# Kernel tuning notes

Measured on AMD Instinct MI355X. Metric: run time of the kernel, lower is better.

The kernel has to match this reference:

```python
import jax, jax.numpy as jnp
import numpy as np
from jax import lax

EPS = 1e-8


def setup_inputs() -> dict:
    key = jax.random.key(0)
    ks = jax.random.split(key, 8)
    B, Cin, Cout, Wd, H, Wi, K = 16, 512, 512, 512, 64, 64, 3
    x = jax.random.normal(ks[0], (B, Cin, H, Wi), dtype=jnp.float32)
    w = jax.random.normal(ks[1], (B, Wd), dtype=jnp.float32)
    noise = jax.random.normal(ks[2], (B, 1, H, Wi), dtype=jnp.float32)
    # EqualizedLinear params (weight stored as N(0,1), runtime scale 1/sqrt(w_dim)); bias init 1.0
    w_style = jax.random.normal(ks[3], (Cin, Wd), dtype=jnp.float32)
    b_style = jnp.ones((Cin,), dtype=jnp.float32)
    # ConvModLayer equalized weight, stored N(0,1), runtime scale 1/sqrt(Cin*K*K)
    w_conv = jax.random.normal(ks[4], (Cout, Cin, K, K), dtype=jnp.float32)
    scale_noise = 0.1 * jax.random.normal(ks[5], (1,), dtype=jnp.float32)
    bias = 0.1 * jax.random.normal(ks[6], (Cout,), dtype=jnp.float32)
    return {"x": x, "w": w, "noise": noise, "w_style": w_style, "b_style": b_style,
            "w_conv": w_conv, "scale_noise": scale_noise, "bias": bias}


def reference(x, w, noise, w_style, b_style, w_conv, scale_noise, bias):
    B, Cin, H, W = x.shape
    Cout, _, K, _ = w_conv.shape
    # to_style: equalized linear, A = w @ (w_style / sqrt(w_dim)).T + b_style
    c_lin = 1.0 / jnp.sqrt(jnp.float32(w_style.shape[1]))
    A = w @ (w_style * c_lin).T + b_style  # [B, Cin]
    # modulated conv (equalized conv weight scale)
    c_conv = 1.0 / jnp.sqrt(jnp.float32(Cin * K * K))
    wts = (w_conv * c_conv)[None] * A[:, None, :, None, None]  # [B, Cout, Cin, K, K]
    demod = lax.rsqrt(jnp.sum(wts * wts, axis=(2, 3, 4), keepdims=True) + EPS)
    wts = wts * demod
    # grouped-conv batch trick: groups = B
    xg = x.reshape(1, B * Cin, H, W)
    wg = wts.reshape(B * Cout, Cin, K, K)
    out = lax.conv_general_dilated(xg, wg, (1, 1), 'SAME',
                                   feature_group_count=B,
                                   dimension_numbers=('NCHW', 'OIHW', 'NCHW'))
    out = out.reshape(B, Cout, H, W)
    out = out + scale_noise[None, :, None, None] * noise
    out = out + bias[None, :, None, None]
    return jnp.where(out >= 0, out, 0.2 * out)  # LeakyReLU(0.2)
```

## Files before the change

### kernel.cpp

```cpp
#include <hip/hip_runtime.h>
#include <stdint.h>


typedef __attribute__((ext_vector_type(8))) short s16x8;
typedef __attribute__((ext_vector_type(4))) float f32x4;

constexpr int CIN = 512, COUT = 512, WD = 512, HW = 4096;
constexpr float C_LIN  = 0.04419417382415922f;
constexpr float C_CONV = 0.014731391274719739f;
constexpr float CC2    = 1.0f / 4608.0f;

constexpr int WSEG = 2432;

constexpr size_t WS_A = 0, WS_S = 32768, WS_DM = 1081344;
constexpr size_t WS_WP = 1310720, WS_XT = 6291456;

__device__ __forceinline__ unsigned short f2bf(float f) {
  union { float f; unsigned int u; } v; v.f = f;
  unsigned int u = v.u + 0x7FFFu + ((v.u >> 16) & 1u);
  return (unsigned short)(u >> 16);
}

__device__ __forceinline__ void gload16(const void* g, void* l) {
  __builtin_amdgcn_global_load_lds((const __attribute__((address_space(1))) void*)g,
                                   (__attribute__((address_space(3))) void*)l, 16, 0, 0);
}

__global__ void k_style(const float* __restrict__ w, const float* __restrict__ wsty,
                        const float* __restrict__ bs, float* __restrict__ A) {
  __shared__ float wl[WD];
  __shared__ float red[256];
  const int ci0 = blockIdx.x * 64, b = blockIdx.y, tid = threadIdx.x;
  for (int i = tid; i < WD; i += 256) wl[i] = w[b * WD + i];
  __syncthreads();
  const int ci_l = tid & 63, part = tid >> 6;
  const float4* row = (const float4*)(wsty + (size_t)(ci0 + ci_l) * WD + part * 128);
  float acc = 0.f;
#pragma unroll
  for (int k = 0; k < 32; ++k) {
    float4 v = row[k];
    acc += v.x * wl[part*128 + 4*k] + v.y * wl[part*128 + 4*k+1]
         + v.z * wl[part*128 + 4*k+2] + v.w * wl[part*128 + 4*k+3];
  }
  red[tid] = acc;
  __syncthreads();
  if (part == 0)
    A[b * CIN + ci0 + ci_l] =
        (red[ci_l] + red[64+ci_l] + red[128+ci_l] + red[192+ci_l]) * C_LIN + bs[ci0 + ci_l];
}

__global__ void k_sw(const float* __restrict__ wc, uint4* __restrict__ wp,
                     float* __restrict__ S) {
  __shared__ float wt[64][289];
  const int ct = blockIdx.x, ch = blockIdx.y, tid = threadIdx.x;
  const int co0 = ct * 64, ci0 = ch * 32;
  for (int i = tid; i < 64 * 288; i += 256) {
    int co = i / 288, r = i - co * 288;
    wt[co][r] = wc[(size_t)(co0 + co) * 4608 + (size_t)ci0 * 9 + r];
  }
  __syncthreads();
  uint4* seg = wp + (size_t)(ct * 16 + ch) * WSEG;
  for (int c = tid; c < 2304; c += 256) {
    int t = c >> 8, rem = c & 255, s = rem >> 6, co = rem & 63;
    union { unsigned short u[8]; uint4 v; } pk;
#pragma unroll
    for (int j = 0; j < 8; ++j) pk.u[j] = f2bf(wt[co][(s*8 + j) * 9 + t] * C_CONV);
    seg[(t * 4 + s) * 66 + co] = pk.v;
  }
  for (int i = tid; i < 2048; i += 256) {
    int co = i >> 5, ci = i & 31;
    float s_ = 0.f;
#pragma unroll
    for (int t = 0; t < 9; ++t) { float v = wt[co][ci * 9 + t]; s_ += v * v; }
    S[(size_t)(co0 + co) * CIN + ci0 + ci] = s_;
  }
}

__global__ void k_demod(const float* __restrict__ S, const float* __restrict__ A,
                        float* __restrict__ dm) {
  __shared__ float a2[CIN];
  __shared__ float red[256];
  const int co0 = blockIdx.x * 32, b = blockIdx.y, tid = threadIdx.x;
  for (int i = tid; i < CIN; i += 256) { float a = A[b * CIN + i]; a2[i] = a * a; }
  __syncthreads();
  const int co_l = tid & 31, part = tid >> 5;
  const float4* row = (const float4*)(S + (size_t)(co0 + co_l) * CIN + part * 64);
  float acc = 0.f;
#pragma unroll
  for (int k = 0; k < 16; ++k) {
    float4 v = row[k];
    acc += v.x * a2[part*64 + 4*k] + v.y * a2[part*64 + 4*k+1]
         + v.z * a2[part*64 + 4*k+2] + v.w * a2[part*64 + 4*k+3];
  }
  red[tid] = acc;
  __syncthreads();
  if (tid < 32) {
    float s_ = 0.f;
#pragma unroll
    for (int p = 0; p < 8; ++p) s_ += red[p * 32 + tid];
    dm[b * COUT + co0 + tid] = rsqrtf(CC2 * s_ + 1e-8f);
  }
}

__global__ void k_xt(const float* __restrict__ x, const float* __restrict__ A,
                     uint4* __restrict__ xt) {
  const int wid = (blockIdx.x << 2) + (threadIdx.x >> 6);
  const int lane = threadIdx.x & 63;
  const int row = wid & 63, ch = (wid >> 6) & 15, b = wid >> 10;
  const float* xb = x + ((size_t)(b * CIN + ch * 32) << 12) + (row << 6) + lane;
  const float* Ab = A + b * CIN + ch * 32;
  uint4* dst = xt + (size_t)((b << 4) + ch) * 16896 + (size_t)(row << 2) * 66;
#pragma unroll
  for (int s = 0; s < 4; ++s) {
    union { unsigned short u[8]; uint4 v; } pk;
#pragma unroll
    for (int j = 0; j < 8; ++j)
      pk.u[j] = f2bf(xb[(size_t)(s * 8 + j) << 12] * Ab[s * 8 + j]);
    dst[s * 66 + 1 + lane] = pk.v;
    if (lane < 2) dst[s * 66 + lane * 65] = (uint4){0, 0, 0, 0};
  }
}

__global__ __launch_bounds__(512, 4) void k_conv(
    const uint4* __restrict__ xt, const uint4* __restrict__ wp,
    const float* __restrict__ demod, const float* __restrict__ noise,
    const float* __restrict__ sn_, const float* __restrict__ bias,
    float* __restrict__ out) {

  __shared__ __align__(16) uint4 x_lds[2640];
  __shared__ __align__(16) uint4 w_lds[WSEG];
  __shared__ float dm_l[64], bi_l[64];

  const int sp = blockIdx.x, ct = blockIdx.y, b = blockIdx.z;
  const int r0 = sp * 8, co0 = ct * 64;
  const int tid = threadIdx.x, lane = tid & 63, wave = tid >> 6;
  const int l15 = lane & 15, l4 = lane >> 4;

  if (tid < 64) dm_l[tid] = demod[b * COUT + co0 + tid];
  else if (tid < 128) bi_l[tid - 64] = bias[co0 + tid - 64];
  if (sp == 0) for (int i = tid; i < 264; i += 512) x_lds[i] = (uint4){0, 0, 0, 0};
  if (sp == 7) for (int i = tid; i < 264; i += 512) x_lds[2376 + i] = (uint4){0, 0, 0, 0};

  const int lo = (r0 - 1 > 0) ? r0 - 1 : 0;
  const int hi = (r0 + 8 < 63) ? r0 + 8 : 63;
  const int cells = (hi - lo + 1) * 264;
  const int dst0 = (lo - (r0 - 1)) * 264;
  const int nI = cells >> 6, tail = cells & 63;

  f32x4 acc[4][4];
#pragma unroll
  for (int m = 0; m < 4; ++m)
#pragma unroll
    for (int f = 0; f < 4; ++f) acc[m][f] = (f32x4){0.f, 0.f, 0.f, 0.f};
  __syncthreads();

  for (int ch = 0; ch < 16; ++ch) {
    const uint4* xsrc = xt + ((size_t)(b * 16 + ch) * 64 + lo) * 264;
    const uint4* wsrc = wp + (size_t)(ct * 16 + ch) * WSEG;
    for (int i = wave; i < nI; i += 8)
      gload16(xsrc + i * 64 + lane, &x_lds[dst0 + i * 64]);
    if (tid < tail) x_lds[dst0 + nI * 64 + tid] = xsrc[nI * 64 + tid];
    for (int i = wave; i < 38; i += 8)
      gload16(wsrc + i * 64 + lane, &w_lds[i * 64]);
    __syncthreads();

#pragma unroll
    for (int t = 0; t < 9; ++t) {
      const int dh = t / 3, dw = t - dh * 3;
      s16x8 afr[4], bfr[4];
#pragma unroll
      for (int m = 0; m < 4; ++m)
        afr[m] = *(const s16x8*)&w_lds[(t * 4 + l4) * 66 + m * 16 + l15];
#pragma unroll
      for (int f = 0; f < 4; ++f)
        bfr[f] = *(const s16x8*)&x_lds[((wave + dh) * 4 + l4) * 66 + f * 16 + l15 + dw];
#pragma unroll
      for (int m = 0; m < 4; ++m)
#pragma unroll
        for (int f = 0; f < 4; ++f)
          acc[m][f] = __builtin_amdgcn_mfma_f32_16x16x32_bf16(afr[m], bfr[f], acc[m][f], 0, 0, 0);
    }
    __syncthreads();
  }

  const float sn = sn_[0];
  const int row = r0 + wave;
  float nz[4];
#pragma unroll
  for (int f = 0; f < 4; ++f) nz[f] = sn * noise[b * HW + row * 64 + f * 16 + l15];
#pragma unroll
  for (int m = 0; m < 4; ++m) {
#pragma unroll
    for (int reg = 0; reg < 4; ++reg) {
      const int co_l = m * 16 + l4 * 4 + reg;
      const float d = dm_l[co_l], bv = bi_l[co_l];
      float* op = out + ((size_t)(b * COUT + co0 + co_l)) * HW + row * 64;
#pragma unroll
      for (int f = 0; f < 4; ++f) {
        float v = d * acc[m][f][reg] + nz[f] + bv;
        op[f * 16 + l15] = (v >= 0.f) ? v : 0.2f * v;
      }
    }
  }
}

extern "C" void kernel_launch(void* const* d_in, const int* in_sizes, int n_in,
                              void* d_out, int out_size, void* d_ws, size_t ws_size,
                              hipStream_t stream) {
  (void)in_sizes; (void)n_in; (void)out_size; (void)ws_size;
  const float* x           = (const float*)d_in[0];
  const float* w           = (const float*)d_in[1];
  const float* noise       = (const float*)d_in[2];
  const float* w_style     = (const float*)d_in[3];
  const float* b_style     = (const float*)d_in[4];
  const float* w_conv      = (const float*)d_in[5];
  const float* scale_noise = (const float*)d_in[6];
  const float* bias        = (const float*)d_in[7];
  float* out = (float*)d_out;

  char* ws = (char*)d_ws;
  float* A     = (float*)(ws + WS_A);
  float* S     = (float*)(ws + WS_S);
  float* demod = (float*)(ws + WS_DM);
  uint4* wpack = (uint4*)(ws + WS_WP);
  uint4* xt    = (uint4*)(ws + WS_XT);

  k_style<<<dim3(8, 16), 256, 0, stream>>>(w, w_style, b_style, A);
  k_sw<<<dim3(8, 16), 256, 0, stream>>>(w_conv, wpack, S);
  k_demod<<<dim3(16, 16), 256, 0, stream>>>(S, A, demod);
  k_xt<<<4096, 256, 0, stream>>>(x, A, xt);
  k_conv<<<dim3(8, 8, 16), 512, 0, stream>>>(xt, wpack, demod, noise, scale_noise, bias, out);
}
```

Measured before the change: 494.5 us.

## Double-buffer conv LDS staging and fuse style/demod into neighbouring kernels

The conv kernel now double-buffers the x and weight LDS tiles, prefetching the next channel chunk while MFMAs run on the current one, and raises wave priority around the MFMA block. The style linear is fused into the x-transform kernel (each block recomputes its 32 style values), and the demodulation reduction moves into the conv prologue, dropping two launches. The weight segment padding is removed. In exchange, doubling LDS lowers occupancy (launch bounds go from 4 to 2 blocks per CU), and the style and demod reductions are recomputed redundantly across blocks.

Result: slower. 546.8 us (+10.6%).

```diff
diff --git a/kernel.cpp b/kernel.cpp
--- a/kernel.cpp
+++ b/kernel.cpp
@@ -10,9 +10,9 @@
 constexpr float C_CONV = 0.014731391274719739f;
 constexpr float CC2    = 1.0f / 4608.0f;
 
-constexpr int WSEG = 2432;
-
-constexpr size_t WS_A = 0, WS_S = 32768, WS_DM = 1081344;
+constexpr int WSEG = 2304;
+
+constexpr size_t WS_A = 0, WS_S = 32768;
 constexpr size_t WS_WP = 1310720, WS_XT = 6291456;
 
 __device__ __forceinline__ unsigned short f2bf(float f) {
@@ -24,29 +24,6 @@
 __device__ __forceinline__ void gload16(const void* g, void* l) {
   __builtin_amdgcn_global_load_lds((const __attribute__((address_space(1))) void*)g,
                                    (__attribute__((address_space(3))) void*)l, 16, 0, 0);
-}
-
-__global__ void k_style(const float* __restrict__ w, const float* __restrict__ wsty,
-                        const float* __restrict__ bs, float* __restrict__ A) {
-  __shared__ float wl[WD];
-  __shared__ float red[256];
-  const int ci0 = blockIdx.x * 64, b = blockIdx.y, tid = threadIdx.x;
-  for (int i = tid; i < WD; i += 256) wl[i] = w[b * WD + i];
-  __syncthreads();
-  const int ci_l = tid & 63, part = tid >> 6;
-  const float4* row = (const float4*)(wsty + (size_t)(ci0 + ci_l) * WD + part * 128);
-  float acc = 0.f;
-#pragma unroll
-  for (int k = 0; k < 32; ++k) {
-    float4 v = row[k];
-    acc += v.x * wl[part*128 + 4*k] + v.y * wl[part*128 + 4*k+1]
-         + v.z * wl[part*128 + 4*k+2] + v.w * wl[part*128 + 4*k+3];
-  }
-  red[tid] = acc;
-  __syncthreads();
-  if (part == 0)
-    A[b * CIN + ci0 + ci_l] =
-        (red[ci_l] + red[64+ci_l] + red[128+ci_l] + red[192+ci_l]) * C_LIN + bs[ci0 + ci_l];
 }
 
 __global__ void k_sw(const float* __restrict__ wc, uint4* __restrict__ wp,
@@ -65,7 +42,7 @@
     union { unsigned short u[8]; uint4 v; } pk;
 #pragma unroll
     for (int j = 0; j < 8; ++j) pk.u[j] = f2bf(wt[co][(s*8 + j) * 9 + t] * C_CONV);
-    seg[(t * 4 + s) * 66 + co] = pk.v;
+    seg[(t * 4 + s) * 64 + co] = pk.v;
   }
   for (int i = tid; i < 2048; i += 256) {
     int co = i >> 5, ci = i & 31;
@@ -76,59 +53,68 @@
   }
 }
 
-__global__ void k_demod(const float* __restrict__ S, const float* __restrict__ A,
-                        float* __restrict__ dm) {
-  __shared__ float a2[CIN];
+__global__ __launch_bounds__(256) void k_xta(
+    const float* __restrict__ x, const float* __restrict__ w,
+    const float* __restrict__ wsty, const float* __restrict__ bs,
+    float* __restrict__ A, uint4* __restrict__ xt) {
+  __shared__ float wl[WD];
   __shared__ float red[256];
-  const int co0 = blockIdx.x * 32, b = blockIdx.y, tid = threadIdx.x;
-  for (int i = tid; i < CIN; i += 256) { float a = A[b * CIN + i]; a2[i] = a * a; }
-  __syncthreads();
-  const int co_l = tid & 31, part = tid >> 5;
-  const float4* row = (const float4*)(S + (size_t)(co0 + co_l) * CIN + part * 64);
-  float acc = 0.f;
-#pragma unroll
-  for (int k = 0; k < 16; ++k) {
-    float4 v = row[k];
-    acc += v.x * a2[part*64 + 4*k] + v.y * a2[part*64 + 4*k+1]
-         + v.z * a2[part*64 + 4*k+2] + v.w * a2[part*64 + 4*k+3];
-  }
-  red[tid] = acc;
-  __syncthreads();
-  if (tid < 32) {
-    float s_ = 0.f;
-#pragma unroll
-    for (int p = 0; p < 8; ++p) s_ += red[p * 32 + tid];
-    dm[b * COUT + co0 + tid] = rsqrtf(CC2 * s_ + 1e-8f);
-  }
-}
-
-__global__ void k_xt(const float* __restrict__ x, const float* __restrict__ A,
-                     uint4* __restrict__ xt) {
-  const int wid = (blockIdx.x << 2) + (threadIdx.x >> 6);
-  const int lane = threadIdx.x & 63;
-  const int row = wid & 63, ch = (wid >> 6) & 15, b = wid >> 10;
-  const float* xb = x + ((size_t)(b * CIN + ch * 32) << 12) + (row << 6) + lane;
-  const float* Ab = A + b * CIN + ch * 32;
-  uint4* dst = xt + (size_t)((b << 4) + ch) * 16896 + (size_t)(row << 2) * 66;
-#pragma unroll
-  for (int s = 0; s < 4; ++s) {
-    union { unsigned short u[8]; uint4 v; } pk;
-#pragma unroll
-    for (int j = 0; j < 8; ++j)
-      pk.u[j] = f2bf(xb[(size_t)(s * 8 + j) << 12] * Ab[s * 8 + j]);
-    dst[s * 66 + 1 + lane] = pk.v;
-    if (lane < 2) dst[s * 66 + lane * 65] = (uint4){0, 0, 0, 0};
-  }
-}
-
-__global__ __launch_bounds__(512, 4) void k_conv(
+  __shared__ float As[32];
+  const int p = blockIdx.x, b = blockIdx.y, tid = threadIdx.x;
+  const int ch = p >> 2, rowgrp = p & 3, ci0 = ch * 32;
+  for (int i = tid; i < WD; i += 256) wl[i] = w[b * WD + i];
+  __syncthreads();
+  const int ci_l = tid >> 3, part = tid & 7;
+  {
+    const float4* row = (const float4*)(wsty + (size_t)(ci0 + ci_l) * WD + part * 64);
+    float acc = 0.f;
+#pragma unroll
+    for (int k = 0; k < 16; ++k) {
+      float4 v = row[k];
+      acc += v.x * wl[part*64 + 4*k] + v.y * wl[part*64 + 4*k+1]
+           + v.z * wl[part*64 + 4*k+2] + v.w * wl[part*64 + 4*k+3];
+    }
+    red[tid] = acc;
+  }
+  __syncthreads();
+  if (part == 0) {
+    float s = 0.f;
+#pragma unroll
+    for (int q = 0; q < 8; ++q) s += red[ci_l * 8 + q];
+    float a = s * C_LIN + bs[ci0 + ci_l];
+    As[ci_l] = a;
+    if (rowgrp == 0) A[b * CIN + ci0 + ci_l] = a;
+  }
+  __syncthreads();
+  const int lane = tid & 63, wave = tid >> 6;
+  const float* xb = x + ((size_t)(b * CIN + ci0) << 12) + lane;
+  uint4* dstb = xt + (size_t)((b << 4) + ch) * 16896;
+#pragma unroll
+  for (int i = 0; i < 4; ++i) {
+    const int rw = rowgrp * 16 + wave * 4 + i;
+    const float* xr = xb + (rw << 6);
+    uint4* dst = dstb + (size_t)(rw * 4) * 66;
+#pragma unroll
+    for (int s = 0; s < 4; ++s) {
+      union { unsigned short u[8]; uint4 v; } pk;
+#pragma unroll
+      for (int j = 0; j < 8; ++j)
+        pk.u[j] = f2bf(xr[(size_t)(s * 8 + j) << 12] * As[s * 8 + j]);
+      dst[s * 66 + 1 + lane] = pk.v;
+      if (lane < 2) dst[s * 66 + lane * 65] = (uint4){0, 0, 0, 0};
+    }
+  }
+}
+
+__global__ __launch_bounds__(512, 2) void k_conv(
     const uint4* __restrict__ xt, const uint4* __restrict__ wp,
-    const float* __restrict__ demod, const float* __restrict__ noise,
-    const float* __restrict__ sn_, const float* __restrict__ bias,
-    float* __restrict__ out) {
-
-  __shared__ __align__(16) uint4 x_lds[2640];
-  __shared__ __align__(16) uint4 w_lds[WSEG];
+    const float* __restrict__ S, const float* __restrict__ A,
+    const float* __restrict__ noise, const float* __restrict__ sn_,
+    const float* __restrict__ bias, float* __restrict__ out) {
+
+  __shared__ __align__(16) uint4 x_lds[2][2640];
+  __shared__ __align__(16) uint4 w_lds[2][WSEG];
+  __shared__ float red[512];
   __shared__ float dm_l[64], bi_l[64];
 
   const int sp = blockIdx.x, ct = blockIdx.y, b = blockIdx.z;
@@ -136,33 +122,62 @@
   const int tid = threadIdx.x, lane = tid & 63, wave = tid >> 6;
   const int l15 = lane & 15, l4 = lane >> 4;
 
-  if (tid < 64) dm_l[tid] = demod[b * COUT + co0 + tid];
-  else if (tid < 128) bi_l[tid - 64] = bias[co0 + tid - 64];
-  if (sp == 0) for (int i = tid; i < 264; i += 512) x_lds[i] = (uint4){0, 0, 0, 0};
-  if (sp == 7) for (int i = tid; i < 264; i += 512) x_lds[2376 + i] = (uint4){0, 0, 0, 0};
-
   const int lo = (r0 - 1 > 0) ? r0 - 1 : 0;
   const int hi = (r0 + 8 < 63) ? r0 + 8 : 63;
   const int cells = (hi - lo + 1) * 264;
   const int dst0 = (lo - (r0 - 1)) * 264;
-  const int nI = cells >> 6, tail = cells & 63;
+
+  auto stage = [&](int buf, int ch) {
+    const uint4* xsrc = xt + ((size_t)(b * 16 + ch) * 64 + lo) * 264;
+    for (int i = wave; i * 64 < cells; i += 8)
+      if (i * 64 + lane < cells)
+        gload16(xsrc + i * 64 + lane, &x_lds[buf][dst0 + i * 64]);
+    const uint4* wsrc = wp + (size_t)(ct * 16 + ch) * WSEG;
+    for (int i = wave; i < 36; i += 8)
+      gload16(wsrc + i * 64 + lane, &w_lds[buf][i * 64]);
+  };
+
+  stage(0, 0);
+
+  if (sp == 0) for (int i = tid; i < 264; i += 512) {
+    x_lds[0][i] = (uint4){0,0,0,0}; x_lds[1][i] = (uint4){0,0,0,0};
+  }
+  if (sp == 7) for (int i = tid; i < 264; i += 512) {
+    x_lds[0][2376+i] = (uint4){0,0,0,0}; x_lds[1][2376+i] = (uint4){0,0,0,0};
+  }
+
+  {
+    const int co = tid >> 3, part = tid & 7;
+    const float4* srow = (const float4*)(S + (size_t)(co0 + co) * CIN + part * 64);
+    const float4* arow = (const float4*)(A + (size_t)b * CIN + part * 64);
+    float acc = 0.f;
+#pragma unroll
+    for (int k = 0; k < 16; ++k) {
+      float4 sv = srow[k], av = arow[k];
+      acc += sv.x*av.x*av.x + sv.y*av.y*av.y + sv.z*av.z*av.z + sv.w*av.w*av.w;
+    }
+    red[tid] = acc;
+  }
+  __syncthreads();
+  if (tid < 64) {
+    float s_ = 0.f;
+#pragma unroll
+    for (int q = 0; q < 8; ++q) s_ += red[tid * 8 + q];
+    dm_l[tid] = rsqrtf(CC2 * s_ + 1e-8f);
+    bi_l[tid] = bias[co0 + tid];
+  }
 
   f32x4 acc[4][4];
 #pragma unroll
   for (int m = 0; m < 4; ++m)
 #pragma unroll
     for (int f = 0; f < 4; ++f) acc[m][f] = (f32x4){0.f, 0.f, 0.f, 0.f};
+
   __syncthreads();
 
   for (int ch = 0; ch < 16; ++ch) {
-    const uint4* xsrc = xt + ((size_t)(b * 16 + ch) * 64 + lo) * 264;
-    const uint4* wsrc = wp + (size_t)(ct * 16 + ch) * WSEG;
-    for (int i = wave; i < nI; i += 8)
-      gload16(xsrc + i * 64 + lane, &x_lds[dst0 + i * 64]);
-    if (tid < tail) x_lds[dst0 + nI * 64 + tid] = xsrc[nI * 64 + tid];
-    for (int i = wave; i < 38; i += 8)
-      gload16(wsrc + i * 64 + lane, &w_lds[i * 64]);
-    __syncthreads();
+    const int buf = ch & 1;
+    if (ch < 15) stage(buf ^ 1, ch + 1);
 
 #pragma unroll
     for (int t = 0; t < 9; ++t) {
@@ -170,15 +185,17 @@
       s16x8 afr[4], bfr[4];
 #pragma unroll
       for (int m = 0; m < 4; ++m)
-        afr[m] = *(const s16x8*)&w_lds[(t * 4 + l4) * 66 + m * 16 + l15];
+        afr[m] = *(const s16x8*)&w_lds[buf][(t * 4 + l4) * 64 + m * 16 + l15];
 #pragma unroll
       for (int f = 0; f < 4; ++f)
-        bfr[f] = *(const s16x8*)&x_lds[((wave + dh) * 4 + l4) * 66 + f * 16 + l15 + dw];
+        bfr[f] = *(const s16x8*)&x_lds[buf][((wave + dh) * 4 + l4) * 66 + f * 16 + l15 + dw];
+      __builtin_amdgcn_s_setprio(1);
 #pragma unroll
       for (int m = 0; m < 4; ++m)
 #pragma unroll
         for (int f = 0; f < 4; ++f)
           acc[m][f] = __builtin_amdgcn_mfma_f32_16x16x32_bf16(afr[m], bfr[f], acc[m][f], 0, 0, 0);
+      __builtin_amdgcn_s_setprio(0);
     }
     __syncthreads();
   }
@@ -221,13 +238,10 @@
   char* ws = (char*)d_ws;
   float* A     = (float*)(ws + WS_A);
   float* S     = (float*)(ws + WS_S);
-  float* demod = (float*)(ws + WS_DM);
   uint4* wpack = (uint4*)(ws + WS_WP);
   uint4* xt    = (uint4*)(ws + WS_XT);
 
-  k_style<<<dim3(8, 16), 256, 0, stream>>>(w, w_style, b_style, A);
   k_sw<<<dim3(8, 16), 256, 0, stream>>>(w_conv, wpack, S);
-  k_demod<<<dim3(16, 16), 256, 0, stream>>>(S, A, demod);
-  k_xt<<<4096, 256, 0, stream>>>(x, A, xt);
-  k_conv<<<dim3(8, 8, 16), 512, 0, stream>>>(xt, wpack, demod, noise, scale_noise, bias, out);
-}
+  k_xta<<<dim3(64, 16), 256, 0, stream>>>(x, w, w_style, b_style, A, xt);
+  k_conv<<<dim3(8, 8, 16), 512, 0, stream>>>(xt, wpack, S, A, noise, scale_noise, bias, out);
+}
```
